# Kernel tuning notes

Hardware: AMD Instinct MI355X
Metric: run time of the kernel (lower is better)

Reference implementation:

```python
import jax, jax.numpy as jnp
import numpy as np

HIDDEN = 1024
N_HEADS = 16
D_HEAD = HIDDEN // N_HEADS


def _rope(q, k):
    # q, k: [B, H, N, d]; interleaved-pair rotation as in the torch module
    B, H, N, d = q.shape
    inv_freq = 1.0 / (10000.0 ** (jnp.arange(0, d, 2, dtype=jnp.float32) / d))  # [d/2]
    pos = jnp.arange(N, dtype=jnp.float32)
    thetas = pos[:, None] * inv_freq[None, :]            # [N, d/2]
    cos, sin = jnp.cos(thetas), jnp.sin(thetas)

    def rot(x):
        xp = x.reshape(B, H, N, d // 2, 2)
        xx, xy = xp[..., 0], xp[..., 1]
        rx = xx * cos - xy * sin
        ry = xx * sin + xy * cos
        return jnp.stack([rx, ry], axis=-1).reshape(B, H, N, d)

    return rot(q), rot(k)


def setup_inputs() -> dict:
    key = jax.random.key(0)
    ks = jax.random.split(key, 9)
    B, N, Hd = 4, 2048, HIDDEN
    s = 1.0 / np.sqrt(Hd)
    return {
        "x": jax.random.normal(ks[0], (B, N, Hd), jnp.float32),
        "Wq": jax.random.normal(ks[1], (Hd, Hd), jnp.float32) * s,
        "bq": jax.random.normal(ks[2], (Hd,), jnp.float32) * 0.02,
        "Wk": jax.random.normal(ks[3], (Hd, Hd), jnp.float32) * s,
        "bk": jax.random.normal(ks[4], (Hd,), jnp.float32) * 0.02,
        "Wv": jax.random.normal(ks[5], (Hd, Hd), jnp.float32) * s,
        "bv": jax.random.normal(ks[6], (Hd,), jnp.float32) * 0.02,
        "Wo": jax.random.normal(ks[7], (Hd, Hd), jnp.float32) * s,
        "bo": jax.random.normal(ks[8], (Hd,), jnp.float32) * 0.02,
    }


def reference(x, Wq, bq, Wk, bk, Wv, bv, Wo, bo):
    B, N, _ = x.shape
    H, d = N_HEADS, D_HEAD
    # torch nn.Linear: y = x @ W.T + b
    q = (x @ Wq.T + bq).reshape(B, N, H, d).transpose(0, 2, 1, 3)  # [B,H,N,d]
    k = (x @ Wk.T + bk).reshape(B, N, H, d).transpose(0, 2, 1, 3)
    v = (x @ Wv.T + bv).reshape(B, N, H, d).transpose(0, 2, 1, 3)
    q, k = _rope(q, k)
    scores = jnp.einsum("bhnd,bhmd->bhnm", q, k) / jnp.sqrt(jnp.asarray(d, x.dtype))
    attn = jax.nn.softmax(scores, axis=-1)
    out = jnp.einsum("bhnm,bhmd->bhnd", attn, v)
    out = out.transpose(0, 2, 1, 3).reshape(B, N, H * d)
    return out @ Wo.T + bo
```

## Files before the change

### kernel.cpp

```cpp
#include <hip/hip_runtime.h>
#include <cmath>

typedef unsigned short u16;
typedef unsigned int u32;
typedef __bf16 bf16_t;
typedef bf16_t bf16x8 __attribute__((ext_vector_type(8)));
typedef float f32x4 __attribute__((ext_vector_type(4)));
typedef u32 u32x4 __attribute__((ext_vector_type(4)));

#define AS1 __attribute__((address_space(1)))
#define AS3 __attribute__((address_space(3)))

__device__ __forceinline__ void g2l16(const void* g, void* l) {
  __builtin_amdgcn_global_load_lds((const AS1 void*)g, (AS3 void*)l, 16, 0, 0);
}

__device__ __forceinline__ u16 f2b(float f) {
  u32 u = __builtin_bit_cast(u32, f);
  u += 0x7FFFu + ((u >> 16) & 1u);
  return (u16)(u >> 16);
}
__device__ __forceinline__ float b2f(u16 h) {
  u32 u = ((u32)h) << 16;
  return __builtin_bit_cast(float, u);
}

__device__ __forceinline__ float exp2fast(float x) {
#if __has_builtin(__builtin_amdgcn_exp2f)
  return __builtin_amdgcn_exp2f(x);
#else
  return exp2f(x);
#endif
}

__device__ __forceinline__ float sin01(float rev) {
#if __has_builtin(__builtin_amdgcn_sinf)
  return __builtin_amdgcn_sinf(rev);
#else
  return __sinf(rev * 6.283185307179586f);
#endif
}
__device__ __forceinline__ float cos01(float rev) {
#if __has_builtin(__builtin_amdgcn_cosf)
  return __builtin_amdgcn_cosf(rev);
#else
  return __cosf(rev * 6.283185307179586f);
#endif
}

__device__ __forceinline__ u32 cvtpk(float lo, float hi) {
  u32 d;
  asm("v_cvt_pk_bf16_f32 %0, %1, %2" : "=v"(d) : "v"(lo), "v"(hi));
  return d;
}

__global__ void mha_f2b_kernel(const float* __restrict__ in, u16* __restrict__ out, int n4) {
  int i = blockIdx.x * blockDim.x + threadIdx.x;
  if (i >= n4) return;
  float4 f = reinterpret_cast<const float4*>(in)[i];
  ushort4 o;
  o.x = f2b(f.x); o.y = f2b(f.y); o.z = f2b(f.z); o.w = f2b(f.w);
  reinterpret_cast<ushort4*>(out)[i] = o;
}

__global__ void mha_f2b4_kernel(const float* __restrict__ a0, const float* __restrict__ a1,
                                const float* __restrict__ a2, const float* __restrict__ a3,
                                u16* __restrict__ o0, u16* __restrict__ o1,
                                u16* __restrict__ o2, u16* __restrict__ o3, int n4) {
  int y = blockIdx.y;
  const float* in = y == 0 ? a0 : y == 1 ? a1 : y == 2 ? a2 : a3;
  u16* out = y == 0 ? o0 : y == 1 ? o1 : y == 2 ? o2 : o3;
  int i = blockIdx.x * blockDim.x + threadIdx.x;
  if (i >= n4) return;
  float4 f = reinterpret_cast<const float4*>(in)[i];
  ushort4 o;
  o.x = f2b(f.x); o.y = f2b(f.y); o.z = f2b(f.z); o.w = f2b(f.w);
  reinterpret_cast<ushort4*>(out)[i] = o;
}

#define BM 128
#define BN 128
#define BK 32

__global__ __launch_bounds__(256) void mha_gemm_bt(
    const u16* __restrict__ A, const u16* __restrict__ Bm,
    const float* __restrict__ bias,
    float* __restrict__ Cf,
    int M, int N, int K)
{
  __shared__ u16 As[BM * BK];
  __shared__ u16 Bs[BN * BK];
  const int tid = threadIdx.x;
  const int wid = tid >> 6, lane = tid & 63;
  const int r16 = lane & 15, g = lane >> 4;
  const int bm = blockIdx.x * BM, bn = blockIdx.y * BN;
  const int wm = (wid >> 1) * 64, wn = (wid & 1) * 64;

  f32x4 acc[4][4] = {};

  const int srow = tid >> 2;
  const int sbyte = (tid & 3) * 16;

  for (int kt = 0; kt < K; kt += BK) {
#pragma unroll
    for (int p = 0; p < 2; ++p) {
      int ra = p * 64 + srow;
      int csw = (sbyte ^ ((ra & 3) << 4)) >> 1;
      g2l16(A  + (size_t)(bm + ra) * K + kt + csw, (u16*)As + p * 2048 + wid * 512);
      g2l16(Bm + (size_t)(bn + ra) * K + kt + csw, (u16*)Bs + p * 2048 + wid * 512);
    }
    __syncthreads();
    bf16x8 af[4], bfr[4];
#pragma unroll
    for (int mf = 0; mf < 4; ++mf) {
      int rr = wm + mf * 16 + r16;
      af[mf] = *reinterpret_cast<const bf16x8*>(&As[rr * 32 + ((g * 8) ^ ((rr & 3) << 3))]);
    }
#pragma unroll
    for (int nf = 0; nf < 4; ++nf) {
      int rr = wn + nf * 16 + r16;
      bfr[nf] = *reinterpret_cast<const bf16x8*>(&Bs[rr * 32 + ((g * 8) ^ ((rr & 3) << 3))]);
    }
    __builtin_amdgcn_s_setprio(1);
#pragma unroll
    for (int mf = 0; mf < 4; ++mf)
#pragma unroll
      for (int nf = 0; nf < 4; ++nf)
        acc[mf][nf] = __builtin_amdgcn_mfma_f32_16x16x32_bf16(af[mf], bfr[nf], acc[mf][nf], 0, 0, 0);
    __builtin_amdgcn_s_setprio(0);
    __syncthreads();
  }

#pragma unroll
  for (int mf = 0; mf < 4; ++mf)
#pragma unroll
    for (int nf = 0; nf < 4; ++nf) {
      int col = bn + wn + nf * 16 + r16;
      float bv = bias[col];
#pragma unroll
      for (int r = 0; r < 4; ++r) {
        int rowm = bm + wm + mf * 16 + g * 4 + r;
        Cf[(size_t)rowm * N + col] = acc[mf][nf][r] + bv;
      }
    }
}

__global__ __launch_bounds__(256) void mha_gemm_qkv(
    const u16* __restrict__ A,
    const u16* __restrict__ W0, const u16* __restrict__ W1, const u16* __restrict__ W2,
    const float* __restrict__ b0, const float* __restrict__ b1, const float* __restrict__ b2,
    u16* __restrict__ C0, u16* __restrict__ C1, u16* __restrict__ Vt,
    int M, int N, int K)
{
  __shared__ u16 As[BM * BK];
  __shared__ u16 Bs[BN * BK];
  const int tid = threadIdx.x;
  const int wid = tid >> 6, lane = tid & 63;
  const int r16 = lane & 15, g = lane >> 4;
  const int by = blockIdx.y;
  const int wsel = by >> 3;
  const u16* Bm = wsel == 0 ? W0 : (wsel == 1 ? W1 : W2);
  const float* bias = wsel == 0 ? b0 : (wsel == 1 ? b1 : b2);
  const int bm = blockIdx.x * BM, bn = (by & 7) * BN;
  const int wm = (wid >> 1) * 64, wn = (wid & 1) * 64;

  f32x4 acc[4][4] = {};

  const int srow = tid >> 2;
  const int sbyte = (tid & 3) * 16;

  for (int kt = 0; kt < K; kt += BK) {
#pragma unroll
    for (int p = 0; p < 2; ++p) {
      int ra = p * 64 + srow;
      int csw = (sbyte ^ ((ra & 3) << 4)) >> 1;
      g2l16(A  + (size_t)(bm + ra) * K + kt + csw, (u16*)As + p * 2048 + wid * 512);
      g2l16(Bm + (size_t)(bn + ra) * K + kt + csw, (u16*)Bs + p * 2048 + wid * 512);
    }
    __syncthreads();
    bf16x8 af[4], bfr[4];
#pragma unroll
    for (int mf = 0; mf < 4; ++mf) {
      int rr = wm + mf * 16 + r16;
      af[mf] = *reinterpret_cast<const bf16x8*>(&As[rr * 32 + ((g * 8) ^ ((rr & 3) << 3))]);
    }
#pragma unroll
    for (int nf = 0; nf < 4; ++nf) {
      int rr = wn + nf * 16 + r16;
      bfr[nf] = *reinterpret_cast<const bf16x8*>(&Bs[rr * 32 + ((g * 8) ^ ((rr & 3) << 3))]);
    }
    __builtin_amdgcn_s_setprio(1);
#pragma unroll
    for (int mf = 0; mf < 4; ++mf)
#pragma unroll
      for (int nf = 0; nf < 4; ++nf)
        acc[mf][nf] = __builtin_amdgcn_mfma_f32_16x16x32_bf16(af[mf], bfr[nf], acc[mf][nf], 0, 0, 0);
    __builtin_amdgcn_s_setprio(0);
    __syncthreads();
  }

  if (wsel == 2) {
#pragma unroll
    for (int mf = 0; mf < 4; ++mf) {
      int rowbase = bm + wm + mf * 16 + g * 4;
      int bb = rowbase >> 11;
      int nb = rowbase & 2047;
#pragma unroll
      for (int nf = 0; nf < 4; ++nf) {
        int col = bn + wn + nf * 16 + r16;
        float bv = bias[col];
        int hh = col >> 6, dd = col & 63;
        u16 w0 = f2b(acc[mf][nf][0] + bv);
        u16 w1 = f2b(acc[mf][nf][1] + bv);
        u16 w2 = f2b(acc[mf][nf][2] + bv);
        u16 w3 = f2b(acc[mf][nf][3] + bv);
        uint2 pkt;
        pkt.x = (u32)w0 | ((u32)w1 << 16);
        pkt.y = (u32)w2 | ((u32)w3 << 16);
        *reinterpret_cast<uint2*>(Vt + ((size_t)((bb * 16 + hh) * 64 + dd)) * 2048 + nb) = pkt;
      }
    }
  } else {
    u16* Cb = wsel == 0 ? C0 : C1;
    const float oscale = wsel == 0 ? 0.18033688011111793f : 1.0f;
#pragma unroll
    for (int nf = 0; nf < 4; ++nf) {
      int col = bn + wn + nf * 16 + r16;
      float bv = bias[col];
      int j = (nf * 16 + r16) >> 1;
      float invj = exp2f(-(float)j * 0.41524101186092503f);
      float invrev = invj * 0.15915494309189535f;
#pragma unroll
      for (int mf = 0; mf < 4; ++mf) {
#pragma unroll
        for (int r = 0; r < 4; ++r) {
          int rowm = bm + wm + mf * 16 + g * 4 + r;
          float v = acc[mf][nf][r] + bv;
          float pv = __shfl_xor(v, 1);
          float rev = (float)(rowm & 2047) * invrev;
          rev -= floorf(rev);
          float sn = sin01(rev), cs = cos01(rev);
          float tt = pv * sn;
          float res = fmaf(v, cs, (r16 & 1) ? tt : -tt);
          Cb[(size_t)rowm * N + col] = f2b(res * oscale);
        }
      }
    }
  }
}

#define QT 256
#define KVT 128
#define NKV 16

__global__ __launch_bounds__(512) void mha_attn_kernel(
    const u16* __restrict__ Q, const u16* __restrict__ Kmat,
    const u16* __restrict__ Vt, u16* __restrict__ Ao)
{
  __shared__ u16 Ks[2][KVT * 64];
  __shared__ u16 Vs[2][64 * KVT];
  const int tid = threadIdx.x;
  const int wid = tid >> 6, lane = tid & 63;
  const int r16 = lane & 15, g = lane >> 4;
  const int bh = blockIdx.x;
  const int b = bh >> 4, h = bh & 15;
  const int q0 = blockIdx.y * QT;
  const int wr = wid * 32;

  const u32x4 onesw = {0x3F803F80u, 0x3F803F80u, 0x3F803F80u, 0x3F803F80u};
  const bf16x8 onesf = __builtin_bit_cast(bf16x8, onesw);

  bf16x8 qf[2][2];
#pragma unroll
  for (int qb = 0; qb < 2; ++qb)
#pragma unroll
    for (int c = 0; c < 2; ++c)
      qf[qb][c] = *reinterpret_cast<const bf16x8*>(
          Q + (size_t)(b * 2048 + q0 + wr + qb * 16 + r16) * 1024 + h * 64 + c * 32 + g * 8);

  f32x4 accO[2][4] = {};
  f32x4 accL[2] = {};

  const int rk = tid >> 3, cbk = (tid & 7) * 16;
  const int rv = tid >> 4, cbv = (tid & 15) * 16;

  auto STAGE = [&](int buf, int j0) {
#pragma unroll
    for (int p = 0; p < 2; ++p) {
      int rr = p * 64 + rk;
      int csw = (cbk ^ ((rr & 7) << 4)) >> 1;
      g2l16(Kmat + (size_t)(b * 2048 + j0 + rr) * 1024 + h * 64 + csw,
            (u16*)Ks[buf] + p * 4096 + wid * 512);
    }
#pragma unroll
    for (int p = 0; p < 2; ++p) {
      int dd = p * 32 + rv;
      int csw = (cbv ^ ((dd & 7) << 4)) >> 1;
      g2l16(Vt + (size_t)(bh * 64 + dd) * 2048 + j0 + csw,
            (u16*)Vs[buf] + p * 4096 + wid * 512);
    }
  };

  STAGE(0, 0);
  __syncthreads();

  for (int t = 0; t < NKV; ++t) {
    const int cur = t & 1;
    if (t + 1 < NKV) STAGE(cur ^ 1, (t + 1) * KVT);

    f32x4 s[2][8] = {};
    const u16* KsC = Ks[cur];
#pragma unroll
    for (int c = 0; c < 2; ++c) {
      bf16x8 kf[8];
#pragma unroll
      for (int nf = 0; nf < 8; ++nf) {
        int rr = nf * 16 + r16;
        int ob = (c * 64 + g * 16) ^ ((rr & 7) << 4);
        kf[nf] = *reinterpret_cast<const bf16x8*>(&KsC[rr * 64 + (ob >> 1)]);
      }
      __builtin_amdgcn_s_setprio(1);
#pragma unroll
      for (int qb = 0; qb < 2; ++qb)
#pragma unroll
        for (int nf = 0; nf < 8; ++nf)
          s[qb][nf] = __builtin_amdgcn_mfma_f32_16x16x32_bf16(kf[nf], qf[qb][c], s[qb][nf], 0, 0, 0);
      __builtin_amdgcn_s_setprio(0);
    }

#pragma unroll
    for (int qb = 0; qb < 2; ++qb)
#pragma unroll
      for (int nf = 0; nf < 8; ++nf)
#pragma unroll
        for (int r = 0; r < 4; ++r)
          s[qb][nf][r] = exp2fast(s[qb][nf][r]);

    bf16x8 pa[2][4];
#pragma unroll
    for (int qb = 0; qb < 2; ++qb)
#pragma unroll
      for (int ks = 0; ks < 4; ++ks) {
        u32 X0 = cvtpk(s[qb][2 * ks][0], s[qb][2 * ks][1]);
        u32 X1 = cvtpk(s[qb][2 * ks][2], s[qb][2 * ks][3]);
        u32 Y0 = cvtpk(s[qb][2 * ks + 1][0], s[qb][2 * ks + 1][1]);
        u32 Y1 = cvtpk(s[qb][2 * ks + 1][2], s[qb][2 * ks + 1][3]);
        asm("v_permlane32_swap_b32 %0, %1" : "+v"(X0), "+v"(Y0));
        asm("v_permlane16_swap_b32 %0, %1" : "+v"(X0), "+v"(Y0));
        asm("v_permlane32_swap_b32 %0, %1" : "+v"(X1), "+v"(Y1));
        asm("v_permlane16_swap_b32 %0, %1" : "+v"(X1), "+v"(Y1));
        u32x4 w = {X0, X1, Y0, Y1};
        pa[qb][ks] = __builtin_bit_cast(bf16x8, w);
      }

    const u16* VsC = Vs[cur];
#pragma unroll
    for (int ks = 0; ks < 4; ++ks) {
      bf16x8 vb[4];
#pragma unroll
      for (int nf = 0; nf < 4; ++nf) {
        int dd = nf * 16 + r16;
        int ob = (ks * 64 + g * 16) ^ ((dd & 7) << 4);
        vb[nf] = *reinterpret_cast<const bf16x8*>(&VsC[dd * 128 + (ob >> 1)]);
      }
      __builtin_amdgcn_s_setprio(1);
#pragma unroll
      for (int qb = 0; qb < 2; ++qb) {
#pragma unroll
        for (int nf = 0; nf < 4; ++nf)
          accO[qb][nf] = __builtin_amdgcn_mfma_f32_16x16x32_bf16(pa[qb][ks], vb[nf], accO[qb][nf], 0, 0, 0);
        accL[qb] = __builtin_amdgcn_mfma_f32_16x16x32_bf16(pa[qb][ks], onesf, accL[qb], 0, 0, 0);
      }
      __builtin_amdgcn_s_setprio(0);
    }
    __syncthreads();
  }

#pragma unroll
  for (int qb = 0; qb < 2; ++qb) {
#pragma unroll
    for (int r = 0; r < 4; ++r) {
      float lb = 1.f / accL[qb][r];
      int rowm = q0 + wr + qb * 16 + g * 4 + r;
#pragma unroll
      for (int nf = 0; nf < 4; ++nf) {
        int dd = nf * 16 + r16;
        Ao[(size_t)(b * 2048 + rowm) * 1024 + h * 64 + dd] = f2b(accO[qb][nf][r] * lb);
      }
    }
  }
}

extern "C" void kernel_launch(void* const* d_in, const int* in_sizes, int n_in,
                              void* d_out, int out_size, void* d_ws, size_t ws_size,
                              hipStream_t stream)
{
  const float* x  = (const float*)d_in[0];
  const float* Wq = (const float*)d_in[1];
  const float* bq = (const float*)d_in[2];
  const float* Wk = (const float*)d_in[3];
  const float* bk = (const float*)d_in[4];
  const float* Wv = (const float*)d_in[5];
  const float* bv = (const float*)d_in[6];
  const float* Wo = (const float*)d_in[7];
  const float* bo = (const float*)d_in[8];
  float* out = (float*)d_out;

  char* ws = (char*)d_ws;
  u16* xb  = (u16*)(ws + 0);
  u16* Wqb = (u16*)(ws + 16777216);
  u16* Wkb = (u16*)(ws + 18874368);
  u16* Wvb = (u16*)(ws + 20971520);
  u16* Wob = (u16*)(ws + 23068672);
  u16* Qb  = (u16*)(ws + 25165824);
  u16* Kb  = (u16*)(ws + 41943040);
  u16* Vtb = (u16*)(ws + 58720256);
  u16* Ab  = (u16*)(ws + 75497472);

  mha_f2b_kernel<<<8192, 256, 0, stream>>>(x, xb, 2097152);
  mha_f2b4_kernel<<<dim3(1024, 4), 256, 0, stream>>>(Wq, Wk, Wv, Wo, Wqb, Wkb, Wvb, Wob, 262144);

  mha_gemm_qkv<<<dim3(64, 24), 256, 0, stream>>>(xb, Wqb, Wkb, Wvb, bq, bk, bv,
                                                 Qb, Kb, Vtb, 8192, 1024, 1024);

  mha_attn_kernel<<<dim3(64, 8), 512, 0, stream>>>(Qb, Kb, Vtb, Ab);

  mha_gemm_bt<<<dim3(64, 8), 256, 0, stream>>>(Ab, Wob, bo, out, 8192, 1024, 1024);
}
```

Before: 208.0 us.

## Double GEMM K-tile to 64 and remap blocks for XCD-aware L2 locality

Both projection GEMMs now stage a 64-wide K slice per iteration, using a wider 8-way XOR swizzle and two MFMA sub-steps per barrier pair. This halves the number of __syncthreads and global-load rounds. The launch grid is flattened to 1D, and block IDs are remapped so consecutive blocks on the same XCD (orig&7) share A rows and W columns, which should improve L2 reuse. LDS use per block doubles to 32KB, which may lower occupancy.

Result: faster. 195.4 us (-6.1%).

```diff
diff --git a/kernel.cpp b/kernel.cpp
--- a/kernel.cpp
+++ b/kernel.cpp
@@ -80,7 +80,7 @@
 
 #define BM 128
 #define BN 128
-#define BK 32
+#define BK 64
 
 __global__ __launch_bounds__(256) void mha_gemm_bt(
     const u16* __restrict__ A, const u16* __restrict__ Bm,
@@ -93,41 +93,48 @@
   const int tid = threadIdx.x;
   const int wid = tid >> 6, lane = tid & 63;
   const int r16 = lane & 15, g = lane >> 4;
-  const int bm = blockIdx.x * BM, bn = blockIdx.y * BN;
+  const int orig = blockIdx.x;
+  const int lid = (orig & 7) * 64 + (orig >> 3);
+  const int bm = (lid >> 3) * BM, bn = (lid & 7) * BN;
   const int wm = (wid >> 1) * 64, wn = (wid & 1) * 64;
 
   f32x4 acc[4][4] = {};
 
-  const int srow = tid >> 2;
-  const int sbyte = (tid & 3) * 16;
+  const int sr = tid >> 3;
+  const int sb = (tid & 7) * 16;
 
   for (int kt = 0; kt < K; kt += BK) {
 #pragma unroll
-    for (int p = 0; p < 2; ++p) {
-      int ra = p * 64 + srow;
-      int csw = (sbyte ^ ((ra & 3) << 4)) >> 1;
+    for (int p = 0; p < 4; ++p) {
+      int ra = p * 32 + sr;
+      int csw = (sb ^ ((ra & 7) << 4)) >> 1;
       g2l16(A  + (size_t)(bm + ra) * K + kt + csw, (u16*)As + p * 2048 + wid * 512);
       g2l16(Bm + (size_t)(bn + ra) * K + kt + csw, (u16*)Bs + p * 2048 + wid * 512);
     }
     __syncthreads();
-    bf16x8 af[4], bfr[4];
-#pragma unroll
-    for (int mf = 0; mf < 4; ++mf) {
-      int rr = wm + mf * 16 + r16;
-      af[mf] = *reinterpret_cast<const bf16x8*>(&As[rr * 32 + ((g * 8) ^ ((rr & 3) << 3))]);
-    }
-#pragma unroll
-    for (int nf = 0; nf < 4; ++nf) {
-      int rr = wn + nf * 16 + r16;
-      bfr[nf] = *reinterpret_cast<const bf16x8*>(&Bs[rr * 32 + ((g * 8) ^ ((rr & 3) << 3))]);
-    }
-    __builtin_amdgcn_s_setprio(1);
-#pragma unroll
-    for (int mf = 0; mf < 4; ++mf)
-#pragma unroll
-      for (int nf = 0; nf < 4; ++nf)
-        acc[mf][nf] = __builtin_amdgcn_mfma_f32_16x16x32_bf16(af[mf], bfr[nf], acc[mf][nf], 0, 0, 0);
-    __builtin_amdgcn_s_setprio(0);
+#pragma unroll
+    for (int c = 0; c < 2; ++c) {
+      bf16x8 af[4], bfr[4];
+#pragma unroll
+      for (int mf = 0; mf < 4; ++mf) {
+        int rr = wm + mf * 16 + r16;
+        int ob = (c * 64 + g * 16) ^ ((rr & 7) << 4);
+        af[mf] = *reinterpret_cast<const bf16x8*>(&As[rr * 64 + (ob >> 1)]);
+      }
+#pragma unroll
+      for (int nf = 0; nf < 4; ++nf) {
+        int rr = wn + nf * 16 + r16;
+        int ob = (c * 64 + g * 16) ^ ((rr & 7) << 4);
+        bfr[nf] = *reinterpret_cast<const bf16x8*>(&Bs[rr * 64 + (ob >> 1)]);
+      }
+      __builtin_amdgcn_s_setprio(1);
+#pragma unroll
+      for (int mf = 0; mf < 4; ++mf)
+#pragma unroll
+        for (int nf = 0; nf < 4; ++nf)
+          acc[mf][nf] = __builtin_amdgcn_mfma_f32_16x16x32_bf16(af[mf], bfr[nf], acc[mf][nf], 0, 0, 0);
+      __builtin_amdgcn_s_setprio(0);
+    }
     __syncthreads();
   }
 
@@ -157,45 +164,52 @@
   const int tid = threadIdx.x;
   const int wid = tid >> 6, lane = tid & 63;
   const int r16 = lane & 15, g = lane >> 4;
-  const int by = blockIdx.y;
-  const int wsel = by >> 3;
+  const int orig = blockIdx.x;
+  const int lid = (orig & 7) * 192 + (orig >> 3);
+  const int wcol = lid % 24;
+  const int wsel = wcol >> 3;
   const u16* Bm = wsel == 0 ? W0 : (wsel == 1 ? W1 : W2);
   const float* bias = wsel == 0 ? b0 : (wsel == 1 ? b1 : b2);
-  const int bm = blockIdx.x * BM, bn = (by & 7) * BN;
+  const int bm = (lid / 24) * BM, bn = (wcol & 7) * BN;
   const int wm = (wid >> 1) * 64, wn = (wid & 1) * 64;
 
   f32x4 acc[4][4] = {};
 
-  const int srow = tid >> 2;
-  const int sbyte = (tid & 3) * 16;
+  const int sr = tid >> 3;
+  const int sb = (tid & 7) * 16;
 
   for (int kt = 0; kt < K; kt += BK) {
 #pragma unroll
-    for (int p = 0; p < 2; ++p) {
-      int ra = p * 64 + srow;
-      int csw = (sbyte ^ ((ra & 3) << 4)) >> 1;
+    for (int p = 0; p < 4; ++p) {
+      int ra = p * 32 + sr;
+      int csw = (sb ^ ((ra & 7) << 4)) >> 1;
       g2l16(A  + (size_t)(bm + ra) * K + kt + csw, (u16*)As + p * 2048 + wid * 512);
       g2l16(Bm + (size_t)(bn + ra) * K + kt + csw, (u16*)Bs + p * 2048 + wid * 512);
     }
     __syncthreads();
-    bf16x8 af[4], bfr[4];
-#pragma unroll
-    for (int mf = 0; mf < 4; ++mf) {
-      int rr = wm + mf * 16 + r16;
-      af[mf] = *reinterpret_cast<const bf16x8*>(&As[rr * 32 + ((g * 8) ^ ((rr & 3) << 3))]);
-    }
-#pragma unroll
-    for (int nf = 0; nf < 4; ++nf) {
-      int rr = wn + nf * 16 + r16;
-      bfr[nf] = *reinterpret_cast<const bf16x8*>(&Bs[rr * 32 + ((g * 8) ^ ((rr & 3) << 3))]);
-    }
-    __builtin_amdgcn_s_setprio(1);
-#pragma unroll
-    for (int mf = 0; mf < 4; ++mf)
-#pragma unroll
-      for (int nf = 0; nf < 4; ++nf)
-        acc[mf][nf] = __builtin_amdgcn_mfma_f32_16x16x32_bf16(af[mf], bfr[nf], acc[mf][nf], 0, 0, 0);
-    __builtin_amdgcn_s_setprio(0);
+#pragma unroll
+    for (int c = 0; c < 2; ++c) {
+      bf16x8 af[4], bfr[4];
+#pragma unroll
+      for (int mf = 0; mf < 4; ++mf) {
+        int rr = wm + mf * 16 + r16;
+        int ob = (c * 64 + g * 16) ^ ((rr & 7) << 4);
+        af[mf] = *reinterpret_cast<const bf16x8*>(&As[rr * 64 + (ob >> 1)]);
+      }
+#pragma unroll
+      for (int nf = 0; nf < 4; ++nf) {
+        int rr = wn + nf * 16 + r16;
+        int ob = (c * 64 + g * 16) ^ ((rr & 7) << 4);
+        bfr[nf] = *reinterpret_cast<const bf16x8*>(&Bs[rr * 64 + (ob >> 1)]);
+      }
+      __builtin_amdgcn_s_setprio(1);
+#pragma unroll
+      for (int mf = 0; mf < 4; ++mf)
+#pragma unroll
+        for (int nf = 0; nf < 4; ++nf)
+          acc[mf][nf] = __builtin_amdgcn_mfma_f32_16x16x32_bf16(af[mf], bfr[nf], acc[mf][nf], 0, 0, 0);
+      __builtin_amdgcn_s_setprio(0);
+    }
     __syncthreads();
   }
 
@@ -420,10 +434,10 @@
   mha_f2b_kernel<<<8192, 256, 0, stream>>>(x, xb, 2097152);
   mha_f2b4_kernel<<<dim3(1024, 4), 256, 0, stream>>>(Wq, Wk, Wv, Wo, Wqb, Wkb, Wvb, Wob, 262144);
 
-  mha_gemm_qkv<<<dim3(64, 24), 256, 0, stream>>>(xb, Wqb, Wkb, Wvb, bq, bk, bv,
-                                                 Qb, Kb, Vtb, 8192, 1024, 1024);
+  mha_gemm_qkv<<<1536, 256, 0, stream>>>(xb, Wqb, Wkb, Wvb, bq, bk, bv,
+                                         Qb, Kb, Vtb, 8192, 1024, 1024);
 
   mha_attn_kernel<<<dim3(64, 8), 512, 0, stream>>>(Qb, Kb, Vtb, Ab);
 
-  mha_gemm_bt<<<dim3(64, 8), 256, 0, stream>>>(Ab, Wob, bo, out, 8192, 1024, 1024);
-}
+  mha_gemm_bt<<<512, 256, 0, stream>>>(Ab, Wob, bo, out, 8192, 1024, 1024);
+}
```
